# Kernel tuning notes

Measured on AMD Instinct MI355X. Metric: run time of the kernel, lower is better.

## Reference

```python
import jax, jax.numpy as jnp
import numpy as np

N = 4096
B = 8192


def setup_inputs() -> dict:
    key = jax.random.key(0)
    kx, kk = jax.random.split(key)
    x = jax.random.normal(kx, (B, N), dtype=jnp.float32)
    kernel = jax.random.normal(kk, (N, N), dtype=jnp.float32)
    return {"x": x, "kernel": kernel}


def reference(x, kernel):
    # Original: matmul(x, diag(diag_part(kernel))).
    # Mathematically identical to scaling column i of x by kernel[i, i];
    # off-diagonal kernel entries never contribute.
    d = jnp.diagonal(kernel)  # [N]
    return x * d  # broadcast over batch -> [B, N]
```

## Files before the change

### kernel.cpp

```cpp
#include <hip/hip_runtime.h>


#define DK_N 4096

typedef float vfloat4 __attribute__((ext_vector_type(4)));

__global__ void dk_extract_diag(const float* __restrict__ k, float* __restrict__ d) {
    int i = blockIdx.x * blockDim.x + threadIdx.x;
    if (i < DK_N) d[i] = k[(size_t)i * (DK_N + 1)];
}

__global__ __launch_bounds__(256) void dk_scale_cols(const vfloat4* __restrict__ x,
                                                     const vfloat4* __restrict__ diag4,
                                                     vfloat4* __restrict__ out,
                                                     int n4) {
    int t = blockIdx.x * blockDim.x + threadIdx.x;
    if (t >= n4) return;
    vfloat4 d = diag4[t & (DK_N / 4 - 1)];
    vfloat4 v = __builtin_nontemporal_load(&x[t]);
    v *= d;
    __builtin_nontemporal_store(v, &out[t]);
}

extern "C" void kernel_launch(void* const* d_in, const int* in_sizes, int n_in,
                              void* d_out, int out_size, void* d_ws, size_t ws_size,
                              hipStream_t stream) {
    const float* x = (const float*)d_in[0];
    const float* kernel = (const float*)d_in[1];
    float* out = (float*)d_out;
    float* diag = (float*)d_ws;

    dk_extract_diag<<<(DK_N + 255) / 256, 256, 0, stream>>>(kernel, diag);

    int n4 = out_size / 4;
    int blocks = (n4 + 255) / 256;
    dk_scale_cols<<<blocks, 256, 0, stream>>>((const vfloat4*)x,
                                              (const vfloat4*)diag,
                                              (vfloat4*)out, n4);
}
```

Before: 246.4 us.

## Fuse diagonal extraction into grid-stride column scaling kernel

Removes the separate diagonal-extraction kernel and workspace round trip. Each thread now reads its four diagonal entries directly from the kernel matrix once, then loops grid-stride over rows with a fixed 2048-block grid. Because the step (524288) is a multiple of 1024 vec4 columns, the column group stays constant per thread. This saves a kernel launch and a dependency, at the cost of four strided gather loads per thread and reduced block count.

```diff
diff --git a/kernel.cpp b/kernel.cpp
--- a/kernel.cpp
+++ b/kernel.cpp
@@ -2,24 +2,31 @@
 
 
 #define DK_N 4096
+#define DK_N4 (DK_N / 4)
 
 typedef float vfloat4 __attribute__((ext_vector_type(4)));
 
-__global__ void dk_extract_diag(const float* __restrict__ k, float* __restrict__ d) {
-    int i = blockIdx.x * blockDim.x + threadIdx.x;
-    if (i < DK_N) d[i] = k[(size_t)i * (DK_N + 1)];
-}
+__global__ __launch_bounds__(256) void dk_scale_cols_fused(
+    const vfloat4* __restrict__ x,
+    const float* __restrict__ kmat,
+    vfloat4* __restrict__ out,
+    int n4) {
+    const int t0 = blockIdx.x * blockDim.x + threadIdx.x;
+    const int step = gridDim.x * blockDim.x;
 
-__global__ __launch_bounds__(256) void dk_scale_cols(const vfloat4* __restrict__ x,
-                                                     const vfloat4* __restrict__ diag4,
-                                                     vfloat4* __restrict__ out,
-                                                     int n4) {
-    int t = blockIdx.x * blockDim.x + threadIdx.x;
-    if (t >= n4) return;
-    vfloat4 d = diag4[t & (DK_N / 4 - 1)];
-    vfloat4 v = __builtin_nontemporal_load(&x[t]);
-    v *= d;
-    __builtin_nontemporal_store(v, &out[t]);
+    const int cg = t0 & (DK_N4 - 1);
+    const int col = cg << 2;
+    vfloat4 d;
+    d.x = kmat[(size_t)(col + 0) * (DK_N + 1)];
+    d.y = kmat[(size_t)(col + 1) * (DK_N + 1)];
+    d.z = kmat[(size_t)(col + 2) * (DK_N + 1)];
+    d.w = kmat[(size_t)(col + 3) * (DK_N + 1)];
+
+    for (int t = t0; t < n4; t += step) {
+        vfloat4 v = __builtin_nontemporal_load(&x[t]);
+        v *= d;
+        __builtin_nontemporal_store(v, &out[t]);
+    }
 }
 
 extern "C" void kernel_launch(void* const* d_in, const int* in_sizes, int n_in,
@@ -28,13 +35,10 @@
     const float* x = (const float*)d_in[0];
     const float* kernel = (const float*)d_in[1];
     float* out = (float*)d_out;
-    float* diag = (float*)d_ws;
-
-    dk_extract_diag<<<(DK_N + 255) / 256, 256, 0, stream>>>(kernel, diag);
+    (void)d_ws; (void)ws_size;
 
     int n4 = out_size / 4;
-    int blocks = (n4 + 255) / 256;
-    dk_scale_cols<<<blocks, 256, 0, stream>>>((const vfloat4*)x,
-                                              (const vfloat4*)diag,
-                                              (vfloat4*)out, n4);
+
+    dk_scale_cols_fused<<<2048, 256, 0, stream>>>(
+        (const vfloat4*)x, kernel, (vfloat4*)out, n4);
 }
```

Result: slower. 258.1 us (+4.7%).
